# Optimization experiments

Measured on AMD Instinct MI355X. Metric: run time of the kernel, lower is better.

## Reference

```python
import jax, jax.numpy as jnp
import numpy as np

BS, D, H, T = 512, 1024, 4096, 64
STEP_SIZE = 0.25
N_INNER = 4  # unit time spacing / STEP_SIZE -> 4 fixed Euler substeps per interval


def setup_inputs() -> dict:
    key = jax.random.key(0)
    k0, k1, k2 = jax.random.split(key, 3)
    scale1 = 1.0 / np.sqrt(D)
    scale2 = 1.0 / np.sqrt(H)
    return {
        "z0": jax.random.normal(k0, (BS, D), jnp.float32),
        "t": jnp.arange(T, dtype=jnp.float32),
        "W1": jax.random.normal(k1, (D, H), jnp.float32) * scale1,
        "b1": jnp.zeros((H,), jnp.float32),
        "W2": jax.random.normal(k2, (H, D), jnp.float32) * scale2,
        "b2": jnp.zeros((D,), jnp.float32),
    }


def reference(z0, t, W1, b1, W2, b2):
    # ODEF func: MLP  f(z) = tanh(z W1 + b1) W2 + b2
    def f(z):
        return jnp.tanh(z @ W1 + b1) @ W2 + b2

    def ode_solve(z, dt):
        # fixed-step Euler over interval dt with N_INNER substeps
        h = dt / N_INNER
        def euler_step(zc, _):
            return zc + h * f(zc), None
        z, _ = jax.lax.scan(euler_step, z, None, length=N_INNER)
        return z

    dts = jnp.abs(t[1:] - t[:-1])  # [T-1]

    def outer(z, dt):
        z_next = ode_solve(z, dt)
        return z_next, z_next

    _, zs = jax.lax.scan(outer, z0, dts)  # zs: [T-1, BS, D]
    # full trajectory, matching ODEAdjoint forward output (return_whole_sequence=True)
    return jnp.concatenate([z0[None], zs], axis=0)  # [T, BS, D]
```

## Files before the change

### kernel.cpp

```cpp
#include <hip/hip_runtime.h>
#include <hip/hip_bf16.h>
#include <stdint.h>

#define BS 512
#define D 1024
#define H 4096
#define T_STEPS 64
#define N_INNER 4
#define SK 4

typedef __attribute__((ext_vector_type(8))) _Float16 f16x8;
typedef __attribute__((ext_vector_type(4))) float f32x4;
typedef __attribute__((ext_vector_type(4))) unsigned short u16x4;
typedef unsigned short u16;

__device__ __forceinline__ u16 f2h_bits(float f) {
    _Float16 h = (_Float16)f;
    return __builtin_bit_cast(u16, h);
}
__device__ __forceinline__ float h2f(u16 b) {
    return (float)__builtin_bit_cast(_Float16, b);
}
__device__ __forceinline__ float fast_tanh(float x) {
    float e = __expf(2.0f * x);
    return 1.0f - 2.0f / (e + 1.0f);
}


__global__ __launch_bounds__(256) void transpose_h(
    const float* __restrict__ src, u16* __restrict__ dst, int rows, int cols) {
    __shared__ float tile[32][33];
    const int tx = threadIdx.x & 31;
    const int ty = threadIdx.x >> 5;
    const int c0 = blockIdx.x * 32, r0 = blockIdx.y * 32;
    #pragma unroll
    for (int i = ty; i < 32; i += 8)
        tile[i][tx] = src[(size_t)(r0 + i) * cols + c0 + tx];
    __syncthreads();
    #pragma unroll
    for (int i = ty; i < 32; i += 8)
        dst[(size_t)(c0 + i) * rows + r0 + tx] = f2h_bits(tile[tx][i]);
}

__global__ __launch_bounds__(256) void transpose_split(
    const float* __restrict__ src, u16* __restrict__ dst_hi,
    u16* __restrict__ dst_lo, int rows, int cols) {
    __shared__ float tile[32][33];
    const int tx = threadIdx.x & 31;
    const int ty = threadIdx.x >> 5;
    const int c0 = blockIdx.x * 32, r0 = blockIdx.y * 32;
    #pragma unroll
    for (int i = ty; i < 32; i += 8)
        tile[i][tx] = src[(size_t)(r0 + i) * cols + c0 + tx];
    __syncthreads();
    #pragma unroll
    for (int i = ty; i < 32; i += 8) {
        const float v = tile[tx][i];
        const u16 hi = f2h_bits(v);
        const u16 lo = f2h_bits(v - h2f(hi));
        const size_t idx = (size_t)(c0 + i) * rows + r0 + tx;
        dst_hi[idx] = hi;
        dst_lo[idx] = lo;
    }
}

__global__ __launch_bounds__(256) void init_z(
    const float* __restrict__ z0, float* __restrict__ z_cur,
    u16* __restrict__ z_h, float* __restrict__ out) {
    const int i = blockIdx.x * 256 + threadIdx.x;
    const float v = z0[i];
    z_cur[i] = v;
    z_h[i] = f2h_bits(v);
    out[i] = v;
}

__device__ __forceinline__ void stage_one(
    const u16* __restrict__ src, u16* lds, int row0, int ldK, int k0, int tid) {
    #pragma unroll
    for (int i = 0; i < 2; ++i) {
        const int L = (i * 256 + tid) * 16;
        const int r = L >> 7;
        const int cb = (L & 127) ^ ((r & 7) << 4);
        const size_t goff = (size_t)(row0 + r) * ldK + k0 + (cb >> 1);
        const int ldsoff = (i * 256 + (tid & ~63)) * 8;
        __builtin_amdgcn_global_load_lds(
            (const __attribute__((address_space(1))) void*)(src + goff),
            (__attribute__((address_space(3))) void*)(lds + ldsoff), 16, 0, 0);
    }
}

__global__ __launch_bounds__(256, 2) void gemm1_step(
    const u16* __restrict__ A_h, const u16* __restrict__ B_w,
    const float* __restrict__ bias, u16* __restrict__ hid_out) {
    __shared__ __align__(16) u16 lA[3][4096];
    __shared__ __align__(16) u16 lB[3][4096];

    const int tid = threadIdx.x;
    const int bid = blockIdx.x;
    const int xcd = bid & 7, loc = bid >> 3;
    const int tn = xcd * 8 + (loc & 7);
    const int tm = loc >> 3;
    const int m0 = tm * 64, n0 = tn * 64;

    const int wave = tid >> 6;
    const int lane = tid & 63;
    const int wr = wave >> 1, wc = wave & 1;
    const int l15 = lane & 15;
    const int lgrp = lane >> 4;
    const int lk8 = lgrp * 8;

    f32x4 acc[2][2];
    #pragma unroll
    for (int mi = 0; mi < 2; ++mi)
        #pragma unroll
        for (int ni = 0; ni < 2; ++ni)
            acc[mi][ni] = (f32x4){0.f, 0.f, 0.f, 0.f};

    auto STAGE = [&](int buf, int kt) {
        const int k0 = kt * 64;
        stage_one(A_h, lA[buf], m0, D, k0, tid);
        stage_one(B_w, lB[buf], n0, D, k0, tid);
    };
    auto COMPUTE = [&](int buf) {
        const char* Ah = (const char*)lA[buf];
        const char* Bh = (const char*)lB[buf];
        #pragma unroll
        for (int kk = 0; kk < 64; kk += 32) {
            f16x8 af[2], bf[2];
            #pragma unroll
            for (int mi = 0; mi < 2; ++mi) {
                const int row = wr * 32 + mi * 16 + l15;
                const int cb = ((kk + lk8) * 2) ^ ((row & 7) << 4);
                af[mi] = *(const f16x8*)(Ah + row * 128 + cb);
            }
            #pragma unroll
            for (int ni = 0; ni < 2; ++ni) {
                const int row = wc * 32 + ni * 16 + l15;
                const int cb = ((kk + lk8) * 2) ^ ((row & 7) << 4);
                bf[ni] = *(const f16x8*)(Bh + row * 128 + cb);
            }
            #pragma unroll
            for (int mi = 0; mi < 2; ++mi)
                #pragma unroll
                for (int ni = 0; ni < 2; ++ni)
                    acc[mi][ni] = __builtin_amdgcn_mfma_f32_16x16x32_f16(
                        af[mi], bf[ni], acc[mi][ni], 0, 0, 0);
        }
    };

    STAGE(0, 0);
    STAGE(1, 1);
    int cur = 0;
    for (int kt = 0; kt < 14; ++kt) {
        asm volatile("s_waitcnt vmcnt(4)" ::: "memory");
        asm volatile("s_barrier" ::: "memory");
        int nb = cur + 2; if (nb >= 3) nb -= 3;
        STAGE(nb, kt + 2);
        COMPUTE(cur);
        ++cur; if (cur == 3) cur = 0;
    }
    asm volatile("s_waitcnt vmcnt(4)" ::: "memory");
    asm volatile("s_barrier" ::: "memory");
    COMPUTE(cur);
    ++cur; if (cur == 3) cur = 0;
    asm volatile("s_waitcnt vmcnt(0)" ::: "memory");
    asm volatile("s_barrier" ::: "memory");
    COMPUTE(cur);

    const int crow_base = m0 + wr * 32;
    const int ccol_base = n0 + wc * 32;
    #pragma unroll
    for (int mi = 0; mi < 2; ++mi)
        #pragma unroll
        for (int ni = 0; ni < 2; ++ni) {
            const int col = ccol_base + ni * 16 + l15;
            const float b = bias[col];
            #pragma unroll
            for (int r = 0; r < 4; ++r) {
                const int row = crow_base + mi * 16 + lgrp * 4 + r;
                const float v = fast_tanh(acc[mi][ni][r] + b);
                hid_out[(size_t)row * H + col] = f2h_bits(v);
            }
        }
}

__global__ __launch_bounds__(256, 2) void gemm2_step(
    const u16* __restrict__ A_h,
    const u16* __restrict__ B_hi, const u16* __restrict__ B_lo,
    float* __restrict__ part) {
    __shared__ __align__(16) u16 lA[3][4096];
    __shared__ __align__(16) u16 lBh[3][4096];
    __shared__ __align__(16) u16 lBl[3][4096];

    const int tid = threadIdx.x;
    const int bid = blockIdx.x;
    const int xcd = bid & 7, loc = bid >> 3;
    const int tn = xcd * 2 + (loc & 1);
    const int tm = (loc >> 1) & 7;
    const int sk = loc >> 4;
    const int m0 = tm * 64, n0 = tn * 64;
    const int k0b = sk * 1024;

    const int wave = tid >> 6;
    const int lane = tid & 63;
    const int wr = wave >> 1, wc = wave & 1;
    const int l15 = lane & 15;
    const int lgrp = lane >> 4;
    const int lk8 = lgrp * 8;

    f32x4 acc[2][2];
    #pragma unroll
    for (int mi = 0; mi < 2; ++mi)
        #pragma unroll
        for (int ni = 0; ni < 2; ++ni)
            acc[mi][ni] = (f32x4){0.f, 0.f, 0.f, 0.f};

    auto STAGE = [&](int buf, int kt) {
        const int k0 = k0b + kt * 64;
        stage_one(A_h,  lA[buf],  m0, H, k0, tid);
        stage_one(B_hi, lBh[buf], n0, H, k0, tid);
        stage_one(B_lo, lBl[buf], n0, H, k0, tid);
    };
    auto COMPUTE = [&](int buf) {
        const char* Ah = (const char*)lA[buf];
        const char* Bh = (const char*)lBh[buf];
        const char* Bl = (const char*)lBl[buf];
        #pragma unroll
        for (int kk = 0; kk < 64; kk += 32) {
            f16x8 af[2], bfh[2], bfl[2];
            #pragma unroll
            for (int mi = 0; mi < 2; ++mi) {
                const int row = wr * 32 + mi * 16 + l15;
                const int cb = ((kk + lk8) * 2) ^ ((row & 7) << 4);
                af[mi] = *(const f16x8*)(Ah + row * 128 + cb);
            }
            #pragma unroll
            for (int ni = 0; ni < 2; ++ni) {
                const int row = wc * 32 + ni * 16 + l15;
                const int cb = ((kk + lk8) * 2) ^ ((row & 7) << 4);
                bfh[ni] = *(const f16x8*)(Bh + row * 128 + cb);
                bfl[ni] = *(const f16x8*)(Bl + row * 128 + cb);
            }
            #pragma unroll
            for (int mi = 0; mi < 2; ++mi)
                #pragma unroll
                for (int ni = 0; ni < 2; ++ni) {
                    acc[mi][ni] = __builtin_amdgcn_mfma_f32_16x16x32_f16(
                        af[mi], bfh[ni], acc[mi][ni], 0, 0, 0);
                    acc[mi][ni] = __builtin_amdgcn_mfma_f32_16x16x32_f16(
                        af[mi], bfl[ni], acc[mi][ni], 0, 0, 0);
                }
        }
    };

    STAGE(0, 0);
    STAGE(1, 1);
    int cur = 0;
    for (int kt = 0; kt < 14; ++kt) {
        asm volatile("s_waitcnt vmcnt(6)" ::: "memory");
        asm volatile("s_barrier" ::: "memory");
        int nb = cur + 2; if (nb >= 3) nb -= 3;
        STAGE(nb, kt + 2);
        COMPUTE(cur);
        ++cur; if (cur == 3) cur = 0;
    }
    asm volatile("s_waitcnt vmcnt(6)" ::: "memory");
    asm volatile("s_barrier" ::: "memory");
    COMPUTE(cur);
    ++cur; if (cur == 3) cur = 0;
    asm volatile("s_waitcnt vmcnt(0)" ::: "memory");
    asm volatile("s_barrier" ::: "memory");
    COMPUTE(cur);

    float* p = part + (size_t)sk * BS * D;
    const int crow_base = m0 + wr * 32;
    const int ccol_base = n0 + wc * 32;
    #pragma unroll
    for (int mi = 0; mi < 2; ++mi)
        #pragma unroll
        for (int ni = 0; ni < 2; ++ni) {
            const int col = ccol_base + ni * 16 + l15;
            #pragma unroll
            for (int r = 0; r < 4; ++r) {
                const int row = crow_base + mi * 16 + lgrp * 4 + r;
                p[(size_t)row * D + col] = acc[mi][ni][r];
            }
        }
}

__global__ __launch_bounds__(256) void reduce_update(
    const float* __restrict__ part, const float* __restrict__ b2,
    const float* __restrict__ z_in, float* __restrict__ z_out,
    u16* __restrict__ zh,
    float* __restrict__ traj, const float* __restrict__ tptr, int iv) {
    const int i = (blockIdx.x * 256 + threadIdx.x) * 4;
    const size_t SZ = (size_t)BS * D;
    const float4 p0 = *(const float4*)(part + i);
    const float4 p1 = *(const float4*)(part + SZ + i);
    const float4 p2 = *(const float4*)(part + 2 * SZ + i);
    const float4 p3 = *(const float4*)(part + 3 * SZ + i);
    const float4 b  = *(const float4*)(b2 + (i & (D - 1)));
    const float4 z  = *(const float4*)(z_in + i);
    const float h = fabsf(tptr[iv + 1] - tptr[iv]) * (1.0f / N_INNER);
    float4 v;
    v.x = z.x + h * (p0.x + p1.x + p2.x + p3.x + b.x);
    v.y = z.y + h * (p0.y + p1.y + p2.y + p3.y + b.y);
    v.z = z.z + h * (p0.z + p1.z + p2.z + p3.z + b.z);
    v.w = z.w + h * (p0.w + p1.w + p2.w + p3.w + b.w);
    *(float4*)(z_out + i) = v;
    u16x4 h4;
    h4.x = f2h_bits(v.x);
    h4.y = f2h_bits(v.y);
    h4.z = f2h_bits(v.z);
    h4.w = f2h_bits(v.w);
    *(u16x4*)(zh + i) = h4;
    if (traj) *(float4*)(traj + i) = v;
}


extern "C" void kernel_launch(void* const* d_in, const int* in_sizes, int n_in,
                              void* d_out, int out_size, void* d_ws, size_t ws_size,
                              hipStream_t stream) {
    const float* z0 = (const float*)d_in[0];
    const float* t  = (const float*)d_in[1];
    const float* W1 = (const float*)d_in[2];
    const float* b1 = (const float*)d_in[3];
    const float* W2 = (const float*)d_in[4];
    const float* b2 = (const float*)d_in[5];
    float* out = (float*)d_out;

    char* ws = (char*)d_ws;
    u16*   W1T    = (u16*)(ws);
    u16*   W2T_hi = (u16*)(ws + (16u << 20));
    u16*   W2T_lo = (u16*)(ws + (24u << 20));
    float* z_cur  = (float*)(ws + (32u << 20));
    u16*   z_h    = (u16*)(ws + (34u << 20));
    u16*   hid_h  = (u16*)(ws + (36u << 20));
    float* part   = (float*)(ws + (44u << 20));

    transpose_h<<<dim3(H / 32, D / 32), 256, 0, stream>>>(W1, W1T, D, H);
    transpose_split<<<dim3(D / 32, H / 32), 256, 0, stream>>>(W2, W2T_hi, W2T_lo, H, D);
    init_z<<<(BS * D) / 256, 256, 0, stream>>>(z0, z_cur, z_h, out);

    for (int iv = 0; iv < T_STEPS - 1; ++iv) {
        for (int s = 0; s < N_INNER; ++s) {
            gemm1_step<<<512, 256, 0, stream>>>(z_h, W1T, b1, hid_h);
            gemm2_step<<<512, 256, 0, stream>>>(hid_h, W2T_hi, W2T_lo, part);
            float* traj = (s == N_INNER - 1) ? out + (size_t)(iv + 1) * BS * D : nullptr;
            reduce_update<<<512, 256, 0, stream>>>(
                part, b2, z_cur, z_cur, z_h, traj, t, iv);
        }
    }
}
```

Baseline: 7.858 ms.

## Retile gemm2 to 128-row tiles with 8-way split-K and double buffering

The second GEMM now uses 128x64 output tiles per block, with four M sub-tiles per wave, and splits K eight ways at 512 each. The staging pipeline changes from three buffers to two, with an extra barrier before each refill, so LDS stays within budget. The reduce kernel loops over SK partial sums, and the workspace offsets are compacted. The larger tiles cut redundant B-fragment loads per MFMA. In exchange, the reduce reads twice as many partial buffers and the shallower pipeline may expose more load latency.

```diff
diff --git a/kernel.cpp b/kernel.cpp
--- a/kernel.cpp
+++ b/kernel.cpp
@@ -7,7 +7,7 @@
 #define H 4096
 #define T_STEPS 64
 #define N_INNER 4
-#define SK 4
+#define SK 8
 
 typedef __attribute__((ext_vector_type(8))) _Float16 f16x8;
 typedef __attribute__((ext_vector_type(4))) float f32x4;
@@ -74,10 +74,11 @@
     out[i] = v;
 }
 
-__device__ __forceinline__ void stage_one(
+template<int NISS>
+__device__ __forceinline__ void stage_rows(
     const u16* __restrict__ src, u16* lds, int row0, int ldK, int k0, int tid) {
     #pragma unroll
-    for (int i = 0; i < 2; ++i) {
+    for (int i = 0; i < NISS; ++i) {
         const int L = (i * 256 + tid) * 16;
         const int r = L >> 7;
         const int cb = (L & 127) ^ ((r & 7) << 4);
@@ -118,8 +119,8 @@
 
     auto STAGE = [&](int buf, int kt) {
         const int k0 = kt * 64;
-        stage_one(A_h, lA[buf], m0, D, k0, tid);
-        stage_one(B_w, lB[buf], n0, D, k0, tid);
+        stage_rows<2>(A_h, lA[buf], m0, D, k0, tid);
+        stage_rows<2>(B_w, lB[buf], n0, D, k0, tid);
     };
     auto COMPUTE = [&](int buf) {
         const char* Ah = (const char*)lA[buf];
@@ -188,18 +189,18 @@
     const u16* __restrict__ A_h,
     const u16* __restrict__ B_hi, const u16* __restrict__ B_lo,
     float* __restrict__ part) {
-    __shared__ __align__(16) u16 lA[3][4096];
-    __shared__ __align__(16) u16 lBh[3][4096];
-    __shared__ __align__(16) u16 lBl[3][4096];
+    __shared__ __align__(16) u16 lA[2][8192];
+    __shared__ __align__(16) u16 lBh[2][4096];
+    __shared__ __align__(16) u16 lBl[2][4096];
 
     const int tid = threadIdx.x;
     const int bid = blockIdx.x;
     const int xcd = bid & 7, loc = bid >> 3;
     const int tn = xcd * 2 + (loc & 1);
-    const int tm = (loc >> 1) & 7;
-    const int sk = loc >> 4;
-    const int m0 = tm * 64, n0 = tn * 64;
-    const int k0b = sk * 1024;
+    const int tm = (loc >> 1) & 3;
+    const int sk = loc >> 3;
+    const int m0 = tm * 128, n0 = tn * 64;
+    const int k0b = sk * 512;
 
     const int wave = tid >> 6;
     const int lane = tid & 63;
@@ -208,18 +209,18 @@
     const int lgrp = lane >> 4;
     const int lk8 = lgrp * 8;
 
-    f32x4 acc[2][2];
-    #pragma unroll
-    for (int mi = 0; mi < 2; ++mi)
+    f32x4 acc[4][2];
+    #pragma unroll
+    for (int mi = 0; mi < 4; ++mi)
         #pragma unroll
         for (int ni = 0; ni < 2; ++ni)
             acc[mi][ni] = (f32x4){0.f, 0.f, 0.f, 0.f};
 
     auto STAGE = [&](int buf, int kt) {
         const int k0 = k0b + kt * 64;
-        stage_one(A_h,  lA[buf],  m0, H, k0, tid);
-        stage_one(B_hi, lBh[buf], n0, H, k0, tid);
-        stage_one(B_lo, lBl[buf], n0, H, k0, tid);
+        stage_rows<4>(A_h,  lA[buf],  m0, H, k0, tid);
+        stage_rows<2>(B_hi, lBh[buf], n0, H, k0, tid);
+        stage_rows<2>(B_lo, lBl[buf], n0, H, k0, tid);
     };
     auto COMPUTE = [&](int buf) {
         const char* Ah = (const char*)lA[buf];
@@ -227,10 +228,10 @@
         const char* Bl = (const char*)lBl[buf];
         #pragma unroll
         for (int kk = 0; kk < 64; kk += 32) {
-            f16x8 af[2], bfh[2], bfl[2];
-            #pragma unroll
-            for (int mi = 0; mi < 2; ++mi) {
-                const int row = wr * 32 + mi * 16 + l15;
+            f16x8 af[4], bfh[2], bfl[2];
+            #pragma unroll
+            for (int mi = 0; mi < 4; ++mi) {
+                const int row = wr * 64 + mi * 16 + l15;
                 const int cb = ((kk + lk8) * 2) ^ ((row & 7) << 4);
                 af[mi] = *(const f16x8*)(Ah + row * 128 + cb);
             }
@@ -242,7 +243,7 @@
                 bfl[ni] = *(const f16x8*)(Bl + row * 128 + cb);
             }
             #pragma unroll
-            for (int mi = 0; mi < 2; ++mi)
+            for (int mi = 0; mi < 4; ++mi)
                 #pragma unroll
                 for (int ni = 0; ni < 2; ++ni) {
                     acc[mi][ni] = __builtin_amdgcn_mfma_f32_16x16x32_f16(
@@ -256,27 +257,23 @@
     STAGE(0, 0);
     STAGE(1, 1);
     int cur = 0;
-    for (int kt = 0; kt < 14; ++kt) {
-        asm volatile("s_waitcnt vmcnt(6)" ::: "memory");
+    for (int kt = 0; kt < 8; ++kt) {
+        if (kt < 7) asm volatile("s_waitcnt vmcnt(8)" ::: "memory");
+        else        asm volatile("s_waitcnt vmcnt(0)" ::: "memory");
         asm volatile("s_barrier" ::: "memory");
-        int nb = cur + 2; if (nb >= 3) nb -= 3;
-        STAGE(nb, kt + 2);
         COMPUTE(cur);
-        ++cur; if (cur == 3) cur = 0;
-    }
-    asm volatile("s_waitcnt vmcnt(6)" ::: "memory");
-    asm volatile("s_barrier" ::: "memory");
-    COMPUTE(cur);
-    ++cur; if (cur == 3) cur = 0;
-    asm volatile("s_waitcnt vmcnt(0)" ::: "memory");
-    asm volatile("s_barrier" ::: "memory");
-    COMPUTE(cur);
+        if (kt < 6) {
+            asm volatile("s_barrier" ::: "memory");
+            STAGE(cur, kt + 2);
+        }
+        cur ^= 1;
+    }
 
     float* p = part + (size_t)sk * BS * D;
-    const int crow_base = m0 + wr * 32;
+    const int crow_base = m0 + wr * 64;
     const int ccol_base = n0 + wc * 32;
     #pragma unroll
-    for (int mi = 0; mi < 2; ++mi)
+    for (int mi = 0; mi < 4; ++mi)
         #pragma unroll
         for (int ni = 0; ni < 2; ++ni) {
             const int col = ccol_base + ni * 16 + l15;
@@ -295,18 +292,20 @@
     float* __restrict__ traj, const float* __restrict__ tptr, int iv) {
     const int i = (blockIdx.x * 256 + threadIdx.x) * 4;
     const size_t SZ = (size_t)BS * D;
-    const float4 p0 = *(const float4*)(part + i);
-    const float4 p1 = *(const float4*)(part + SZ + i);
-    const float4 p2 = *(const float4*)(part + 2 * SZ + i);
-    const float4 p3 = *(const float4*)(part + 3 * SZ + i);
-    const float4 b  = *(const float4*)(b2 + (i & (D - 1)));
-    const float4 z  = *(const float4*)(z_in + i);
+    float4 s = *(const float4*)(part + i);
+    #pragma unroll
+    for (int k = 1; k < SK; ++k) {
+        const float4 pk = *(const float4*)(part + (size_t)k * SZ + i);
+        s.x += pk.x; s.y += pk.y; s.z += pk.z; s.w += pk.w;
+    }
+    const float4 b = *(const float4*)(b2 + (i & (D - 1)));
+    const float4 z = *(const float4*)(z_in + i);
     const float h = fabsf(tptr[iv + 1] - tptr[iv]) * (1.0f / N_INNER);
     float4 v;
-    v.x = z.x + h * (p0.x + p1.x + p2.x + p3.x + b.x);
-    v.y = z.y + h * (p0.y + p1.y + p2.y + p3.y + b.y);
-    v.z = z.z + h * (p0.z + p1.z + p2.z + p3.z + b.z);
-    v.w = z.w + h * (p0.w + p1.w + p2.w + p3.w + b.w);
+    v.x = z.x + h * (s.x + b.x);
+    v.y = z.y + h * (s.y + b.y);
+    v.z = z.z + h * (s.z + b.z);
+    v.w = z.w + h * (s.w + b.w);
     *(float4*)(z_out + i) = v;
     u16x4 h4;
     h4.x = f2h_bits(v.x);
@@ -331,12 +330,12 @@
 
     char* ws = (char*)d_ws;
     u16*   W1T    = (u16*)(ws);
-    u16*   W2T_hi = (u16*)(ws + (16u << 20));
-    u16*   W2T_lo = (u16*)(ws + (24u << 20));
-    float* z_cur  = (float*)(ws + (32u << 20));
-    u16*   z_h    = (u16*)(ws + (34u << 20));
-    u16*   hid_h  = (u16*)(ws + (36u << 20));
-    float* part   = (float*)(ws + (44u << 20));
+    u16*   W2T_hi = (u16*)(ws + (8u << 20));
+    u16*   W2T_lo = (u16*)(ws + (16u << 20));
+    float* z_cur  = (float*)(ws + (24u << 20));
+    u16*   z_h    = (u16*)(ws + (26u << 20));
+    u16*   hid_h  = (u16*)(ws + (28u << 20));
+    float* part   = (float*)(ws + (32u << 20));
 
     transpose_h<<<dim3(H / 32, D / 32), 256, 0, stream>>>(W1, W1T, D, H);
     transpose_split<<<dim3(D / 32, H / 32), 256, 0, stream>>>(W2, W2T_hi, W2T_lo, H, D);
```

New measurement: 7.527 ms. -4.2%, faster.
